# Performance work log

Hardware: AMD Instinct MI355X
Metric: run time of the kernel (lower is better)

The kernel has to match this reference:

```python
import jax, jax.numpy as jnp
import numpy as np

N_HEAD = 16

def setup_inputs() -> dict:
    key = jax.random.key(0)
    ks = jax.random.split(key, 5)
    C = 1024
    x = jax.random.normal(ks[0], (2, 2048, C), dtype=jnp.float32)
    W_qkv = jax.random.normal(ks[1], (C, 3 * C), dtype=jnp.float32) * (C ** -0.5)
    b_qkv = jnp.zeros((3 * C,), dtype=jnp.float32)
    W_proj = jax.random.normal(ks[2], (C, C), dtype=jnp.float32) * (C ** -0.5)
    b_proj = jnp.zeros((C,), dtype=jnp.float32)
    return {"x": x, "W_qkv": W_qkv, "b_qkv": b_qkv, "W_proj": W_proj, "b_proj": b_proj}

def reference(x, W_qkv, b_qkv, W_proj, b_proj):
    B, T, C = x.shape
    H = N_HEAD
    D = C // H
    scale = D ** -0.5
    qkv = x @ W_qkv + b_qkv                      # [B,T,3C]
    q, k, v = jnp.split(qkv, 3, axis=-1)
    # [B,T,C] -> [B,H,T,D]
    q = q.reshape(B, T, H, D).transpose(0, 2, 1, 3)
    k = k.reshape(B, T, H, D).transpose(0, 2, 1, 3)
    v = v.reshape(B, T, H, D).transpose(0, 2, 1, 3)
    attn = jnp.einsum('bhqd,bhkd->bhqk', q, k) * scale   # [B,H,T,T]
    causal = jnp.tril(jnp.ones((T, T), dtype=bool))
    attn = jnp.where(causal, attn, -jnp.inf)
    attn = jax.nn.softmax(attn, axis=-1)
    y = jnp.einsum('bhqk,bhkd->bhqd', attn, v)           # [B,H,T,D]
    y = y.transpose(0, 2, 1, 3).reshape(B, T, C)
    return y @ W_proj + b_proj
```

## Files before the change

kernel.cpp:

```cpp
#include <hip/hip_runtime.h>

typedef __attribute__((ext_vector_type(8))) _Float16 h8;
typedef __attribute__((ext_vector_type(4))) float f4;

#define QKSCALE 0.18033688011112042f

__global__ __launch_bounds__(256) void cast_f16_kernel(const float* __restrict__ in,
                                                       _Float16* __restrict__ out, int n) {
  int i = (blockIdx.x * 256 + threadIdx.x) * 8;
  if (i >= n) return;
  const float4* p = (const float4*)(in + i);
  float4 a = p[0], b = p[1];
  h8 v;
  v[0] = (_Float16)a.x; v[1] = (_Float16)a.y; v[2] = (_Float16)a.z; v[3] = (_Float16)a.w;
  v[4] = (_Float16)b.x; v[5] = (_Float16)b.y; v[6] = (_Float16)b.z; v[7] = (_Float16)b.w;
  *(h8*)(out + i) = v;
}

__global__ __launch_bounds__(256) void transp_cast_kernel(const float* __restrict__ W,
                                                          _Float16* __restrict__ Wt, int K, int N) {
  __shared__ _Float16 tile[64][72];
  int k0 = blockIdx.y * 64, n0 = blockIdx.x * 64;
  int t = threadIdx.x;
#pragma unroll
  for (int i = 0; i < 16; ++i) {
    int idx = i * 256 + t;
    int kr = idx >> 6, nc = idx & 63;
    tile[kr][nc] = (_Float16)W[(size_t)(k0 + kr) * N + n0 + nc];
  }
  __syncthreads();
#pragma unroll
  for (int i = 0; i < 2; ++i) {
    int idx = i * 256 + t;
    int nr = idx >> 3, kc = (idx & 7) * 8;
    h8 v;
#pragma unroll
    for (int j = 0; j < 8; ++j) v[j] = tile[kc + j][nr];
    *(h8*)&Wt[(size_t)(n0 + nr) * K + k0 + kc] = v;
  }
}

template <int MODE>
__global__ __launch_bounds__(256) void gemm_f16(const _Float16* __restrict__ A,
                                                const _Float16* __restrict__ Bt,
                                                const float* __restrict__ bias,
                                                float* __restrict__ outF,
                                                _Float16* __restrict__ oQ,
                                                _Float16* __restrict__ oK,
                                                _Float16* __restrict__ oV,
                                                int M, int N, int K) {
  __shared__ _Float16 As[128 * 64];
  __shared__ _Float16 Bs[128 * 64];
  const int m0 = blockIdx.y * 128, n0 = blockIdx.x * 128;
  const int tid = threadIdx.x;
  const int wave = tid >> 6, lane = tid & 63;
  const int wr = (wave >> 1) * 64, wc = (wave & 1) * 64;
  const int lrow = lane & 15, g = lane >> 4;
  f4 acc[4][4];
  const f4 z4 = {0.f, 0.f, 0.f, 0.f};
#pragma unroll
  for (int m = 0; m < 4; ++m)
#pragma unroll
    for (int n = 0; n < 4; ++n) acc[m][n] = z4;

  for (int k0 = 0; k0 < K; k0 += 64) {
#pragma unroll
    for (int i = 0; i < 4; ++i) {
      int L = i * 256 + tid;
      int row = L >> 3, c = L & 7;
      int cs = (c ^ (row & 7)) * 8;
      *(h8*)&As[row * 64 + c * 8] = *(const h8*)&A[(size_t)(m0 + row) * K + k0 + cs];
      *(h8*)&Bs[row * 64 + c * 8] = *(const h8*)&Bt[(size_t)(n0 + row) * K + k0 + cs];
    }
    __syncthreads();
#pragma unroll
    for (int ss = 0; ss < 2; ++ss) {
      h8 af[4], bf[4];
#pragma unroll
      for (int m = 0; m < 4; ++m) {
        int row = wr + m * 16 + lrow;
        af[m] = *(const h8*)&As[row * 64 + (((ss * 4 + g) ^ (row & 7)) * 8)];
      }
#pragma unroll
      for (int n = 0; n < 4; ++n) {
        int row = wc + n * 16 + lrow;
        bf[n] = *(const h8*)&Bs[row * 64 + (((ss * 4 + g) ^ (row & 7)) * 8)];
      }
#pragma unroll
      for (int m = 0; m < 4; ++m)
#pragma unroll
        for (int n = 0; n < 4; ++n)
          acc[m][n] = __builtin_amdgcn_mfma_f32_16x16x32_f16(af[m], bf[n], acc[m][n], 0, 0, 0);
    }
    __syncthreads();
  }

#pragma unroll
  for (int n = 0; n < 4; ++n) {
    const int gcol = n0 + wc + n * 16 + lrow;
    const float bv = bias ? bias[gcol] : 0.f;
#pragma unroll
    for (int m = 0; m < 4; ++m) {
#pragma unroll
      for (int r = 0; r < 4; ++r) {
        const int grow = m0 + wr + m * 16 + g * 4 + r;
        float v = acc[m][n][r] + bv;
        if (MODE == 0) {
          outF[(size_t)grow * N + gcol] = v;
        } else {
          int part = gcol >> 10;
          int c1 = gcol & 1023;
          int hh = c1 >> 6, d = c1 & 63;
          int b = grow >> 11, t = grow & 2047;
          int bh = b * 16 + hh;
          if (part == 0)
            oQ[((size_t)bh * 2048 + t) * 64 + d] = (_Float16)(v * QKSCALE);
          else if (part == 1)
            oK[((size_t)bh * 2048 + t) * 64 + d] = (_Float16)v;
          else
            oV[((size_t)bh * 64 + d) * 2048 + t] = (_Float16)v;
        }
      }
    }
  }
}

__global__ __launch_bounds__(256) void attn_kernel(const _Float16* __restrict__ Qg,
                                                   const _Float16* __restrict__ Kg,
                                                   const _Float16* __restrict__ Vtg,
                                                   _Float16* __restrict__ Og) {
  __shared__ _Float16 slab[4][32][72];
  __shared__ float mlds[2][4][32];

  const int idx = blockIdx.x;
  const int bh = (idx & 7) | (((idx >> 3) & 3) << 3);
  const int qt2 = 63 - (idx >> 5);
  const int q0 = qt2 * 32;

  const int wave = threadIdx.x >> 6, lane = threadIdx.x & 63;
  const int lrow = lane & 15, g = lane >> 4;
  const int b = bh >> 4, h = bh & 15;
  const _Float16* Q = Qg + (size_t)bh * 2048 * 64;
  const _Float16* K = Kg + (size_t)bh * 2048 * 64;
  const _Float16* Vt = Vtg + (size_t)bh * 64 * 2048;

  h8 aq[2][2];
#pragma unroll
  for (int mt = 0; mt < 2; ++mt)
#pragma unroll
    for (int ss = 0; ss < 2; ++ss)
      aq[mt][ss] = *(const h8*)&Q[(q0 + mt * 16 + lrow) * 64 + ss * 32 + g * 8];

  const f4 z4 = {0.f, 0.f, 0.f, 0.f};
  f4 o[2][4];
#pragma unroll
  for (int mt = 0; mt < 2; ++mt)
#pragma unroll
    for (int dt = 0; dt < 4; ++dt) o[mt][dt] = z4;
  float mrow[2][4], lpart[2][4];
#pragma unroll
  for (int mt = 0; mt < 2; ++mt)
#pragma unroll
    for (int r = 0; r < 4; ++r) { mrow[mt][r] = -1e30f; lpart[mt][r] = 0.f; }

  _Float16(*pw)[72] = slab[wave];
  const int NT = (qt2 >> 1) + 1;

  for (int it = wave; it < NT; it += 4) {
    const int kv0 = it * 64;
    h8 kf[4][2];
#pragma unroll
    for (int ct = 0; ct < 4; ++ct)
#pragma unroll
      for (int ss = 0; ss < 2; ++ss)
        kf[ct][ss] = *(const h8*)&K[(kv0 + ct * 16 + lrow) * 64 + ss * 32 + g * 8];

    f4 s[2][4];
#pragma unroll
    for (int mt = 0; mt < 2; ++mt)
#pragma unroll
      for (int ct = 0; ct < 4; ++ct) s[mt][ct] = z4;
#pragma unroll
    for (int ss = 0; ss < 2; ++ss)
#pragma unroll
      for (int mt = 0; mt < 2; ++mt)
#pragma unroll
        for (int ct = 0; ct < 4; ++ct)
          s[mt][ct] = __builtin_amdgcn_mfma_f32_16x16x32_f16(aq[mt][ss], kf[ct][ss], s[mt][ct], 0, 0, 0);

    h8 vf[4][2];
#pragma unroll
    for (int dt = 0; dt < 4; ++dt)
#pragma unroll
      for (int ss = 0; ss < 2; ++ss)
        vf[dt][ss] = *(const h8*)&Vt[(size_t)(dt * 16 + lrow) * 2048 + kv0 + ss * 32 + g * 8];

    if (it == NT - 1) {
#pragma unroll
      for (int mt = 0; mt < 2; ++mt)
#pragma unroll
        for (int ct = 0; ct < 4; ++ct)
#pragma unroll
          for (int r = 0; r < 4; ++r)
            if (kv0 + ct * 16 + lrow > q0 + mt * 16 + g * 4 + r) s[mt][ct][r] = -1e30f;
    }

    float pm[2][4];
    bool need = false;
#pragma unroll
    for (int mt = 0; mt < 2; ++mt)
#pragma unroll
      for (int r = 0; r < 4; ++r) {
        pm[mt][r] = fmaxf(fmaxf(s[mt][0][r], s[mt][1][r]), fmaxf(s[mt][2][r], s[mt][3][r]));
        need = need || (pm[mt][r] > mrow[mt][r] + 8.f);
      }
    if (__any(need)) {
#pragma unroll
      for (int mt = 0; mt < 2; ++mt)
#pragma unroll
        for (int r = 0; r < 4; ++r) {
          float m = pm[mt][r];
          m = fmaxf(m, __shfl_xor(m, 1));
          m = fmaxf(m, __shfl_xor(m, 2));
          m = fmaxf(m, __shfl_xor(m, 4));
          m = fmaxf(m, __shfl_xor(m, 8));
          float mn = fmaxf(mrow[mt][r], m);
          float fr = __builtin_amdgcn_exp2f(mrow[mt][r] - mn);
          mrow[mt][r] = mn;
          lpart[mt][r] *= fr;
#pragma unroll
          for (int dt = 0; dt < 4; ++dt) o[mt][dt][r] *= fr;
        }
    }
#pragma unroll
    for (int mt = 0; mt < 2; ++mt)
#pragma unroll
      for (int r = 0; r < 4; ++r) {
        float ps = 0.f;
#pragma unroll
        for (int ct = 0; ct < 4; ++ct) {
          float p = __builtin_amdgcn_exp2f(s[mt][ct][r] - mrow[mt][r]);
          ps += p;
          pw[mt * 16 + g * 4 + r][ct * 16 + lrow] = (_Float16)p;
        }
        lpart[mt][r] += ps;
      }

    h8 ap[2][2];
#pragma unroll
    for (int mt = 0; mt < 2; ++mt)
#pragma unroll
      for (int ss = 0; ss < 2; ++ss)
        ap[mt][ss] = *(const h8*)&pw[mt * 16 + lrow][ss * 32 + g * 8];

#pragma unroll
    for (int ss = 0; ss < 2; ++ss)
#pragma unroll
      for (int mt = 0; mt < 2; ++mt)
#pragma unroll
        for (int dt = 0; dt < 4; ++dt)
          o[mt][dt] = __builtin_amdgcn_mfma_f32_16x16x32_f16(ap[mt][ss], vf[dt][ss], o[mt][dt], 0, 0, 0);
  }

#pragma unroll
  for (int mt = 0; mt < 2; ++mt)
#pragma unroll
    for (int r = 0; r < 4; ++r) {
      float l = lpart[mt][r];
      l += __shfl_xor(l, 1);
      l += __shfl_xor(l, 2);
      l += __shfl_xor(l, 4);
      l += __shfl_xor(l, 8);
      lpart[mt][r] = l;
    }

  if (lrow == 0) {
#pragma unroll
    for (int mt = 0; mt < 2; ++mt)
#pragma unroll
      for (int r = 0; r < 4; ++r) {
        mlds[0][wave][mt * 16 + g * 4 + r] = mrow[mt][r];
        mlds[1][wave][mt * 16 + g * 4 + r] = lpart[mt][r];
      }
  }
#pragma unroll
  for (int mt = 0; mt < 2; ++mt)
#pragma unroll
    for (int r = 0; r < 4; ++r) {
      float inv = lpart[mt][r] > 0.f ? 1.f / lpart[mt][r] : 0.f;
#pragma unroll
      for (int dt = 0; dt < 4; ++dt)
        pw[mt * 16 + g * 4 + r][dt * 16 + lrow] = (_Float16)(o[mt][dt][r] * inv);
    }
  __syncthreads();

  {
    const int ql = threadIdx.x >> 3;
    const int d0 = (threadIdx.x & 7) * 8;
    float m0 = mlds[0][0][ql], m1 = mlds[0][1][ql], m2 = mlds[0][2][ql], m3 = mlds[0][3][ql];
    float M = fmaxf(fmaxf(m0, m1), fmaxf(m2, m3));
    float f0 = __builtin_amdgcn_exp2f(m0 - M) * mlds[1][0][ql];
    float f1 = __builtin_amdgcn_exp2f(m1 - M) * mlds[1][1][ql];
    float f2 = __builtin_amdgcn_exp2f(m2 - M) * mlds[1][2][ql];
    float f3 = __builtin_amdgcn_exp2f(m3 - M) * mlds[1][3][ql];
    float inv = 1.f / (f0 + f1 + f2 + f3);
    h8 o0 = *(const h8*)&slab[0][ql][d0];
    h8 o1 = *(const h8*)&slab[1][ql][d0];
    h8 o2 = *(const h8*)&slab[2][ql][d0];
    h8 o3 = *(const h8*)&slab[3][ql][d0];
    h8 outv;
#pragma unroll
    for (int j = 0; j < 8; ++j) {
      float v = f0 * (float)o0[j] + f1 * (float)o1[j] + f2 * (float)o2[j] + f3 * (float)o3[j];
      outv[j] = (_Float16)(v * inv);
    }
    *(h8*)&Og[((size_t)b * 2048 + q0 + ql) * 1024 + h * 64 + d0] = outv;
  }
}

extern "C" void kernel_launch(void* const* d_in, const int* in_sizes, int n_in,
                              void* d_out, int out_size, void* d_ws, size_t ws_size,
                              hipStream_t stream) {
  const float* x = (const float*)d_in[0];
  const float* Wqkv = (const float*)d_in[1];
  const float* bqkv = (const float*)d_in[2];
  const float* Wproj = (const float*)d_in[3];
  const float* bproj = (const float*)d_in[4];
  float* out = (float*)d_out;

  char* ws = (char*)d_ws;
  const size_t MB = 1u << 20;
  _Float16* xh     = (_Float16*)(ws + 0 * MB);
  _Float16* wqkvt  = (_Float16*)(ws + 8 * MB);
  _Float16* wprojt = (_Float16*)(ws + 14 * MB);
  _Float16* qh     = (_Float16*)(ws + 16 * MB);
  _Float16* kh     = (_Float16*)(ws + 24 * MB);
  _Float16* vth    = (_Float16*)(ws + 32 * MB);
  _Float16* oh     = (_Float16*)(ws + 40 * MB);

  cast_f16_kernel<<<2048, 256, 0, stream>>>(x, xh, 4194304);
  transp_cast_kernel<<<dim3(48, 16), 256, 0, stream>>>(Wqkv, wqkvt, 1024, 3072);
  transp_cast_kernel<<<dim3(16, 16), 256, 0, stream>>>(Wproj, wprojt, 1024, 1024);

  gemm_f16<1><<<dim3(24, 32), 256, 0, stream>>>(xh, wqkvt, bqkv, nullptr, qh, kh, vth,
                                                4096, 3072, 1024);
  attn_kernel<<<dim3(2048), 256, 0, stream>>>(qh, kh, vth, oh);
  gemm_f16<0><<<dim3(8, 32), 256, 0, stream>>>(oh, wprojt, bproj, out, nullptr, nullptr, nullptr,
                                               4096, 1024, 1024);
}
```

Before: 161.1 us.

## Use direct global-to-LDS loads, MFMA priority hints, and vectorized V-transpose stores

The GEMM tile loads now use global_load_lds to move data straight from global memory into shared memory, skipping the round trip through registers. The destination is linear per thread while the source column is XOR-swizzled, which keeps the existing swizzle layout. s_setprio raises wave priority around the MFMA blocks in both the GEMM and the attention kernels. The V output of the QKV GEMM is written as 4-wide half vectors along t instead of scalar strided stores. Risks are the ordering and wait semantics of global_load_lds before __syncthreads, and gains that may be small if the kernels are not bound by these costs.

After: 152.8 us. 1.05x faster.

```diff
diff --git a/kernel.cpp b/kernel.cpp
--- a/kernel.cpp
+++ b/kernel.cpp
@@ -1,9 +1,15 @@
 #include <hip/hip_runtime.h>
 
 typedef __attribute__((ext_vector_type(8))) _Float16 h8;
+typedef __attribute__((ext_vector_type(4))) _Float16 h4;
 typedef __attribute__((ext_vector_type(4))) float f4;
 
 #define QKSCALE 0.18033688011112042f
+
+__device__ __forceinline__ void gload16(const void* g, void* l) {
+  __builtin_amdgcn_global_load_lds((const __attribute__((address_space(1))) void*)g,
+                                   (__attribute__((address_space(3))) void*)l, 16, 0, 0);
+}
 
 __global__ __launch_bounds__(256) void cast_f16_kernel(const float* __restrict__ in,
                                                        _Float16* __restrict__ out, int n) {
@@ -56,6 +62,9 @@
   const int wave = tid >> 6, lane = tid & 63;
   const int wr = (wave >> 1) * 64, wc = (wave & 1) * 64;
   const int lrow = lane & 15, g = lane >> 4;
+
+  const int row_ = tid >> 3, c_ = tid & 7;
+
   f4 acc[4][4];
   const f4 z4 = {0.f, 0.f, 0.f, 0.f};
 #pragma unroll
@@ -66,11 +75,11 @@
   for (int k0 = 0; k0 < K; k0 += 64) {
 #pragma unroll
     for (int i = 0; i < 4; ++i) {
-      int L = i * 256 + tid;
-      int row = L >> 3, c = L & 7;
-      int cs = (c ^ (row & 7)) * 8;
-      *(h8*)&As[row * 64 + c * 8] = *(const h8*)&A[(size_t)(m0 + row) * K + k0 + cs];
-      *(h8*)&Bs[row * 64 + c * 8] = *(const h8*)&Bt[(size_t)(n0 + row) * K + k0 + cs];
+      int row = i * 32 + row_;
+      int cs = (c_ ^ (row & 7)) * 8;
+      int ldst = (i * 256 + tid) * 8;
+      gload16(&A[(size_t)(m0 + row) * K + k0 + cs], &As[ldst]);
+      gload16(&Bt[(size_t)(n0 + row) * K + k0 + cs], &Bs[ldst]);
     }
     __syncthreads();
 #pragma unroll
@@ -86,11 +95,13 @@
         int row = wc + n * 16 + lrow;
         bf[n] = *(const h8*)&Bs[row * 64 + (((ss * 4 + g) ^ (row & 7)) * 8)];
       }
+      __builtin_amdgcn_s_setprio(1);
 #pragma unroll
       for (int m = 0; m < 4; ++m)
 #pragma unroll
         for (int n = 0; n < 4; ++n)
           acc[m][n] = __builtin_amdgcn_mfma_f32_16x16x32_f16(af[m], bf[n], acc[m][n], 0, 0, 0);
+      __builtin_amdgcn_s_setprio(0);
     }
     __syncthreads();
   }
@@ -99,26 +110,38 @@
   for (int n = 0; n < 4; ++n) {
     const int gcol = n0 + wc + n * 16 + lrow;
     const float bv = bias ? bias[gcol] : 0.f;
-#pragma unroll
-    for (int m = 0; m < 4; ++m) {
-#pragma unroll
-      for (int r = 0; r < 4; ++r) {
-        const int grow = m0 + wr + m * 16 + g * 4 + r;
-        float v = acc[m][n][r] + bv;
-        if (MODE == 0) {
-          outF[(size_t)grow * N + gcol] = v;
-        } else {
-          int part = gcol >> 10;
-          int c1 = gcol & 1023;
-          int hh = c1 >> 6, d = c1 & 63;
-          int b = grow >> 11, t = grow & 2047;
-          int bh = b * 16 + hh;
-          if (part == 0)
-            oQ[((size_t)bh * 2048 + t) * 64 + d] = (_Float16)(v * QKSCALE);
-          else if (part == 1)
-            oK[((size_t)bh * 2048 + t) * 64 + d] = (_Float16)v;
-          else
-            oV[((size_t)bh * 64 + d) * 2048 + t] = (_Float16)v;
+    if (MODE == 1 && (gcol >> 10) == 2) {
+      const int c1 = gcol & 1023;
+      const int hh = c1 >> 6, d = c1 & 63;
+#pragma unroll
+      for (int m = 0; m < 4; ++m) {
+        const int grow = m0 + wr + m * 16 + g * 4;
+        const int b = grow >> 11, t = grow & 2047;
+        h4 pv;
+#pragma unroll
+        for (int r = 0; r < 4; ++r) pv[r] = (_Float16)(acc[m][n][r] + bv);
+        *(h4*)&oV[(((size_t)(b * 16 + hh)) * 64 + d) * 2048 + t] = pv;
+      }
+    } else {
+#pragma unroll
+      for (int m = 0; m < 4; ++m) {
+#pragma unroll
+        for (int r = 0; r < 4; ++r) {
+          const int grow = m0 + wr + m * 16 + g * 4 + r;
+          float v = acc[m][n][r] + bv;
+          if (MODE == 0) {
+            outF[(size_t)grow * N + gcol] = v;
+          } else {
+            int part = gcol >> 10;
+            int c1 = gcol & 1023;
+            int hh = c1 >> 6, d = c1 & 63;
+            int b = grow >> 11, t = grow & 2047;
+            int bh = b * 16 + hh;
+            if (part == 0)
+              oQ[((size_t)bh * 2048 + t) * 64 + d] = (_Float16)(v * QKSCALE);
+            else
+              oK[((size_t)bh * 2048 + t) * 64 + d] = (_Float16)v;
+          }
         }
       }
     }
@@ -180,6 +203,7 @@
     for (int mt = 0; mt < 2; ++mt)
 #pragma unroll
       for (int ct = 0; ct < 4; ++ct) s[mt][ct] = z4;
+    __builtin_amdgcn_s_setprio(1);
 #pragma unroll
     for (int ss = 0; ss < 2; ++ss)
 #pragma unroll
@@ -187,6 +211,7 @@
 #pragma unroll
         for (int ct = 0; ct < 4; ++ct)
           s[mt][ct] = __builtin_amdgcn_mfma_f32_16x16x32_f16(aq[mt][ss], kf[ct][ss], s[mt][ct], 0, 0, 0);
+    __builtin_amdgcn_s_setprio(0);
 
     h8 vf[4][2];
 #pragma unroll
@@ -253,6 +278,7 @@
       for (int ss = 0; ss < 2; ++ss)
         ap[mt][ss] = *(const h8*)&pw[mt * 16 + lrow][ss * 32 + g * 8];
 
+    __builtin_amdgcn_s_setprio(1);
 #pragma unroll
     for (int ss = 0; ss < 2; ++ss)
 #pragma unroll
@@ -260,6 +286,7 @@
 #pragma unroll
         for (int dt = 0; dt < 4; ++dt)
           o[mt][dt] = __builtin_amdgcn_mfma_f32_16x16x32_f16(ap[mt][ss], vf[dt][ss], o[mt][dt], 0, 0, 0);
+    __builtin_amdgcn_s_setprio(0);
   }
 
 #pragma unroll
```
